# Performance work log

Hardware: AMD Instinct MI355X
Metric: run time of the kernel (lower is better)

The kernel has to match this reference:

```python
import jax, jax.numpy as jnp
import numpy as np

N_NODES = 4194304  # 2**22
LEVELS = 10
COARSE = 8192
RANK = 2
NNZ = 8388608


def _interp_linear(u, N):
    """torch F.interpolate(mode='linear', align_corners=False) along axis 1. u: (B,M,R) -> (B,N,R)."""
    M = u.shape[1]
    pos = (jnp.arange(N, dtype=jnp.float32) + 0.5) * (M / N) - 0.5
    pos = jnp.clip(pos, 0.0, M - 1)
    i0 = jnp.floor(pos).astype(jnp.int32)
    i1 = jnp.minimum(i0 + 1, M - 1)
    w = (pos - i0.astype(jnp.float32))[None, :, None]
    return u[:, i0] * (1.0 - w) + u[:, i1] * w


def _apply_hodlr(diag, u_factors, v_factors, x):
    B, N, _ = x.shape
    y = diag * x
    L = u_factors.shape[0]
    for lvl in range(L):
        num_splits = 2 ** (lvl + 1)
        bs = N // num_splits
        if bs == 0:
            continue
        uc, vc = u_factors[lvl], v_factors[lvl]
        u_full = _interp_linear(uc, N) if uc.shape[1] != N else uc
        v_full = _interp_linear(vc, N) if vc.shape[1] != N else vc
        P = num_splits // 2
        valid = P * 2 * bs
        xv = x[:, :valid].reshape(B, P, 2, bs, 1)
        uv = u_full[:, :valid].reshape(B, P, 2, bs, -1)
        vv = v_full[:, :valid].reshape(B, P, 2, bs, -1)
        xL, xR = xv[:, :, 0], xv[:, :, 1]
        uL, uR = uv[:, :, 0], uv[:, :, 1]
        vL, vR = vv[:, :, 0], vv[:, :, 1]
        xRp = jnp.einsum('bpkr,bpko->bpro', vR, xR)  # (B,P,R,1)
        xLp = jnp.einsum('bpkr,bpko->bpro', vL, xL)
        yL = jnp.einsum('bpkr,bpro->bpko', uL, xRp)  # (B,P,bs,1)
        yR = jnp.einsum('bpkr,bpro->bpko', uR, xLp)
        upd = jnp.stack([yL, yR], axis=2).reshape(B, valid, 1)
        if valid < N:
            upd = jnp.pad(upd, ((0, 0), (0, N - valid), (0, 0)))
        y = y + upd
    return y


def setup_inputs() -> dict:
    key = jax.random.key(0)
    ks = jax.random.split(key, 6)
    diag = jax.random.uniform(ks[0], (1, N_NODES, 1), dtype=jnp.float32)
    u_factors = jax.random.normal(ks[1], (LEVELS, 1, COARSE, RANK), dtype=jnp.float32)
    v_factors = jax.random.normal(ks[2], (LEVELS, 1, COARSE, RANK), dtype=jnp.float32)
    A_values = jax.random.normal(ks[3], (NNZ,), dtype=jnp.float32)
    z = jax.random.normal(ks[4], (1, N_NODES, 1), dtype=jnp.float32)
    A_indices = jax.random.randint(ks[5], (2, NNZ), 0, N_NODES, dtype=jnp.int64) if jax.config.jax_enable_x64 else jax.random.randint(ks[5], (2, NNZ), 0, N_NODES, dtype=jnp.int32)
    return {"diag": diag, "u_factors": u_factors, "v_factors": v_factors,
            "A_values": A_values, "z": z, "A_indices": A_indices, "num_nodes": N_NODES}


def reference(diag, u_factors, v_factors, A_values, z, A_indices, num_nodes):
    N = num_nodes
    w = _apply_hodlr(diag, u_factors, v_factors, z)          # (1,N,1)
    w_flat = w.reshape(N)
    rows, cols = A_indices[0], A_indices[1]
    y_flat = jax.ops.segment_sum(A_values * w_flat[cols], rows, num_segments=N)
    y = y_flat.reshape(1, N, 1)
    loss = jnp.mean((y - z) ** 2)
    return loss
```

## Files before the change

kernel.cpp:

```cpp
#include <hip/hip_runtime.h>

#define N_NODES 4194304
#define LEVELS  10
#define COARSE  8192
#define NNZ_E   8388608
#define NB      256
#define CB_SZ   16384
#define RB_SZ   16384
#define HB      1024
#define EPB     8192
#define TILE    8192
#define CAPC    34816u
#define CAPR    34816u

typedef int          v4i __attribute__((ext_vector_type(4)));
typedef float        v4f __attribute__((ext_vector_type(4)));
typedef unsigned int v4u __attribute__((ext_vector_type(4)));
typedef unsigned int v2u __attribute__((ext_vector_type(2)));

static __device__ __forceinline__ unsigned short f2bf(float x) {
    unsigned u = __float_as_uint(x);
    return (unsigned short)((u + 0x7FFFu + ((u >> 16) & 1u)) >> 16);
}
static __device__ __forceinline__ float bf2f(unsigned short h) {
    return __uint_as_float((unsigned)h << 16);
}
static __device__ __forceinline__ unsigned f18(float p) {
    return ((__float_as_uint(p) + 0x2000u) >> 14) & 0x3FFFFu;
}

__global__ __launch_bounds__(512) void kA(const float* __restrict__ z,
                                          float2* __restrict__ M,
                                          float* __restrict__ S,
                                          float* __restrict__ out,
                                          unsigned* __restrict__ colCtr,
                                          unsigned* __restrict__ rowCtr) {
    int b = blockIdx.x, t = threadIdx.x;
    if (b == 0) {
        for (int i = t; i < 2046 * 2; i += 512) S[i] = 0.f;
        if (t == 0) out[0] = 0.f;
        if (t < 256) {
            colCtr[t] = (unsigned)t * CAPC;
            rowCtr[t] = (unsigned)t * CAPR;
        }
    }
    int lane = t & 63, wave = t >> 6;
    int chunk = b * 8 + wave;
    int base = chunk * 256 + lane * 4;
    float4 zv = *(const float4*)(z + base);
    float a0 = 0.f, a1 = 0.f;
    const float* zp = (const float*)&zv;
#pragma unroll
    for (int j = 0; j < 4; ++j) {
        float p = ((float)(base + j) + 0.5f) * (1.0f / 512.0f) - 0.5f;
        p = fminf(fmaxf(p, 0.0f), (float)(COARSE - 1));
        float f = p - floorf(p);
        a0 += zp[j] * (1.0f - f);
        a1 += zp[j] * f;
    }
#pragma unroll
    for (int off = 32; off >= 1; off >>= 1) {
        a0 += __shfl_xor(a0, off, 64);
        a1 += __shfl_xor(a1, off, 64);
    }
    if (lane == 0) M[chunk] = make_float2(a0, a1);
}

__global__ __launch_bounds__(256) void kB(const float2* __restrict__ M,
                                          const float* __restrict__ V,
                                          float* __restrict__ S) {
    int b = blockIdx.x, t = threadIdx.x;
    int lvl = b >> 3, slice = b & 7;
    const float2* Vl = (const float2*)(V + lvl * COARSE * 2);
    float s0 = 0.f, s1 = 0.f;
    int c0 = slice * 2048 + t * 8;
#pragma unroll
    for (int cc = 0; cc < 8; ++cc) {
        int c = c0 + cc;
        float2 m = M[c];
        int k = (c > 0) ? ((c - 1) >> 1) : 0;
        int kp = min(k + 1, COARSE - 1);
        float2 vk = Vl[k], vkp = Vl[kp];
        s0 += vk.x * m.x + vkp.x * m.y;
        s1 += vk.y * m.x + vkp.y * m.y;
    }
    int gw = min(1 << (10 - lvl), 64);
    for (int sh = gw >> 1; sh >= 1; sh >>= 1) {
        s0 += __shfl_xor(s0, sh, 64);
        s1 += __shfl_xor(s1, sh, 64);
    }
    if ((t & (gw - 1)) == 0) {
        int bb = c0 >> (13 - lvl);
        int soff = (2 << lvl) - 2;
        unsafeAtomicAdd(&S[(soff + bb) * 2 + 0], s0);
        unsafeAtomicAdd(&S[(soff + bb) * 2 + 1], s1);
    }
}

__global__ __launch_bounds__(512) void kC(const float* __restrict__ diag,
                                          const float* __restrict__ z,
                                          const float* __restrict__ S,
                                          const float* __restrict__ U,
                                          unsigned short* __restrict__ wb,
                                          const int* __restrict__ rows,
                                          const int* __restrict__ cols,
                                          const float* __restrict__ vals,
                                          unsigned* __restrict__ colCtr,
                                          v2u* __restrict__ colBinned) {
    int b = blockIdx.x, t = threadIdx.x;
    if (b < 2048) {
        int tid = b * 512 + t;
        int base = tid * 4;
        int c = base >> 8;
        int k = (c > 0) ? ((c - 1) >> 1) : 0;
        int kp = min(k + 1, COARSE - 1);
        float g0 = 0.f, g1 = 0.f;
#pragma unroll
        for (int lvl = 0; lvl < LEVELS; ++lvl) {
            int sib = (c >> (13 - lvl)) ^ 1;
            int soff = (2 << lvl) - 2;
            float2 s2 = ((const float2*)S)[soff + sib];
            const float2* Ul = (const float2*)(U + lvl * COARSE * 2);
            float2 uk = Ul[k], ukp = Ul[kp];
            g0 += uk.x * s2.x + uk.y * s2.y;
            g1 += ukp.x * s2.x + ukp.y * s2.y;
        }
        float4 d4 = *(const float4*)(diag + base);
        float4 z4 = *(const float4*)(z + base);
        const float* dp = (const float*)&d4;
        const float* zp = (const float*)&z4;
        ushort4 h4;
        unsigned short* hp = (unsigned short*)&h4;
#pragma unroll
        for (int j = 0; j < 4; ++j) {
            float p = ((float)(base + j) + 0.5f) * (1.0f / 512.0f) - 0.5f;
            p = fminf(fmaxf(p, 0.0f), (float)(COARSE - 1));
            float f = p - floorf(p);
            hp[j] = f2bf(dp[j] * zp[j] + (g0 + f * (g1 - g0)));
        }
        *(ushort4*)(wb + base) = h4;
    } else {
        __shared__ v2u sortedP[EPB];
        __shared__ unsigned cur[NB], gb[NB];
        __shared__ unsigned wsum[4], wbase[4];
        int blk = b - 2048;
        int base = blk * EPB;
        v4i r[4], c[4];
        v4f v[4];
#pragma unroll
        for (int j = 0; j < 4; ++j) {
            int e = base + j * 2048 + t * 4;
            r[j] = __builtin_nontemporal_load((const v4i*)(rows + e));
            c[j] = __builtin_nontemporal_load((const v4i*)(cols + e));
            v[j] = __builtin_nontemporal_load((const v4f*)(vals + e));
        }
        if (t < 256) cur[t] = 0u;
        __syncthreads();
#pragma unroll
        for (int j = 0; j < 4; ++j) {
            atomicAdd(&cur[c[j].x >> 14], 1u);
            atomicAdd(&cur[c[j].y >> 14], 1u);
            atomicAdd(&cur[c[j].z >> 14], 1u);
            atomicAdd(&cur[c[j].w >> 14], 1u);
        }
        __syncthreads();
        unsigned lv = (t < 256) ? cur[t] : 0u;
        unsigned lincl = lv;
        if (t < 256) {
#pragma unroll
            for (int off = 1; off < 64; off <<= 1) {
                unsigned n = __shfl_up(lincl, off, 64);
                if ((t & 63) >= off) lincl += n;
            }
            if ((t & 63) == 63) wsum[t >> 6] = lincl;
        }
        __syncthreads();
        if (t == 0) {
            unsigned a = 0;
            for (int i = 0; i < 4; ++i) { wbase[i] = a; a += wsum[i]; }
        }
        __syncthreads();
        if (t < 256) {
            unsigned lexcl = wbase[t >> 6] + lincl - lv;
            gb[t] = atomicAdd(&colCtr[t], lv) - lexcl;
            cur[t] = lexcl;
        }
        __syncthreads();
#pragma unroll
        for (int j = 0; j < 4; ++j) {
            const int* rp = (const int*)&r[j];
            const int* cp = (const int*)&c[j];
            const float* vp = (const float*)&v[j];
#pragma unroll
            for (int kk = 0; kk < 4; ++kk) {
                int row = rp[kk], col = cp[kk];
                unsigned cb = (unsigned)col >> 14;
                unsigned cl = (unsigned)col & 16383u;
                v2u ent;
                ent.x = (unsigned)row | ((cl & 0x3FFu) << 22);
                ent.y = (cl >> 10) | (cb << 4) | ((unsigned)f2bf(vp[kk]) << 16);
                unsigned i = atomicAdd(&cur[cb], 1u);
                sortedP[i] = ent;
            }
        }
        __syncthreads();
#pragma unroll
        for (int k = 0; k < 16; ++k) {
            int i = k * 512 + t;
            v2u e = sortedP[i];
            unsigned bkt = (e.y >> 4) & 0xFFu;
            __builtin_nontemporal_store(e, colBinned + gb[bkt] + i);
        }
    }
}

__global__ __launch_bounds__(512) void kD(const unsigned short* __restrict__ wb,
                                          const v2u* __restrict__ colBinned,
                                          const unsigned* __restrict__ colCtr,
                                          unsigned* __restrict__ rowCtr,
                                          unsigned* __restrict__ packed) {
    __shared__ unsigned short wSl[CB_SZ];
    __shared__ unsigned sortedP[TILE];
    __shared__ unsigned char sortedB[TILE];
    __shared__ unsigned cur[NB], gb[NB];
    __shared__ unsigned wsum[4], wbase[4];
    int b = blockIdx.x >> 1, h = blockIdx.x & 1, t = threadIdx.x;

    unsigned s0 = (unsigned)b * CAPC;
    unsigned n = colCtr[b] - s0;
    const v4u* wg = (const v4u*)(wb + (size_t)b * CB_SZ);
    for (int i = t; i < CB_SZ / 8; i += 512) ((v4u*)wSl)[i] = wg[i];
    __syncthreads();

    for (unsigned t0 = (unsigned)h * TILE; t0 < n; t0 += 2u * TILE) {
        unsigned cnt = min((unsigned)TILE, n - t0);
        v2u ev[16];
#pragma unroll
        for (int k = 0; k < 16; ++k) {
            unsigned i = (unsigned)(k * 512 + t);
            if (i < cnt) ev[k] = __builtin_nontemporal_load(colBinned + s0 + t0 + i);
        }
        if (t < 256) cur[t] = 0u;
        __syncthreads();
#pragma unroll
        for (int k = 0; k < 16; ++k) {
            if ((unsigned)(k * 512 + t) < cnt)
                atomicAdd(&cur[(ev[k].x & 0x3FFFFFu) >> 14], 1u);
        }
        __syncthreads();
        unsigned lv = (t < 256) ? cur[t] : 0u;
        unsigned lincl = lv;
        if (t < 256) {
#pragma unroll
            for (int off = 1; off < 64; off <<= 1) {
                unsigned nn = __shfl_up(lincl, off, 64);
                if ((t & 63) >= off) lincl += nn;
            }
            if ((t & 63) == 63) wsum[t >> 6] = lincl;
        }
        __syncthreads();
        if (t == 0) {
            unsigned a = 0;
            for (int i = 0; i < 4; ++i) { wbase[i] = a; a += wsum[i]; }
        }
        __syncthreads();
        if (t < 256) {
            unsigned lexcl = wbase[t >> 6] + lincl - lv;
            gb[t] = atomicAdd(&rowCtr[t], lv) - lexcl;
            cur[t] = lexcl;
        }
        __syncthreads();
#pragma unroll
        for (int k = 0; k < 16; ++k) {
            if ((unsigned)(k * 512 + t) < cnt) {
                v2u e = ev[k];
                unsigned row = e.x & 0x3FFFFFu;
                unsigned cl = (e.x >> 22) | ((e.y & 0xFu) << 10);
                float p = bf2f((unsigned short)(e.y >> 16)) * bf2f(wSl[cl]);
                unsigned rb = row >> 14;
                unsigned i = atomicAdd(&cur[rb], 1u);
                sortedP[i] = ((row & 16383u) << 18) | f18(p);
                sortedB[i] = (unsigned char)rb;
            }
        }
        __syncthreads();
#pragma unroll
        for (int k = 0; k < 16; ++k) {
            unsigned i = (unsigned)(k * 512 + t);
            if (i < cnt) {
                unsigned bkt = sortedB[i];
                __builtin_nontemporal_store(sortedP[i], packed + gb[bkt] + i);
            }
        }
        __syncthreads();
    }
}

__global__ __launch_bounds__(1024) void kE(const unsigned* __restrict__ packed,
                                           const unsigned* __restrict__ rowCtr,
                                           const float* __restrict__ z,
                                           float* __restrict__ out) {
    __shared__ float acc[RB_SZ];
    __shared__ float red[16];
    int b = blockIdx.x, t = threadIdx.x;

    unsigned s0 = (unsigned)b * CAPR;
    unsigned n = rowCtr[b] - s0;
    for (int i = t; i < RB_SZ / 4; i += 1024) ((float4*)acc)[i] = make_float4(0.f, 0.f, 0.f, 0.f);
    __syncthreads();

    for (unsigned i = t; i < n; i += 1024) {
        unsigned e = __builtin_nontemporal_load(packed + s0 + i);
        atomicAdd(&acc[e >> 18], __uint_as_float((e & 0x3FFFFu) << 14));
    }
    __syncthreads();

    float part = 0.f;
    int gbase = b * RB_SZ;
    for (int i = t; i < RB_SZ; i += 1024) {
        float d = acc[i] - z[gbase + i];
        part += d * d;
    }
#pragma unroll
    for (int off = 32; off >= 1; off >>= 1) part += __shfl_xor(part, off, 64);
    if ((t & 63) == 0) red[t >> 6] = part;
    __syncthreads();
    if (t == 0) {
        float s = 0.f;
        for (int i = 0; i < 16; ++i) s += red[i];
        unsafeAtomicAdd(out, s * (1.0f / (float)N_NODES));
    }
}

extern "C" void kernel_launch(void* const* d_in, const int* in_sizes, int n_in,
                              void* d_out, int out_size, void* d_ws, size_t ws_size,
                              hipStream_t stream) {
    const float* diag  = (const float*)d_in[0];
    const float* U     = (const float*)d_in[1];
    const float* V     = (const float*)d_in[2];
    const float* Avals = (const float*)d_in[3];
    const float* z     = (const float*)d_in[4];
    const int*   Aidx  = (const int*)d_in[5];
    const int* rows = Aidx;
    const int* cols = Aidx + NNZ_E;

    char* ws = (char*)d_ws;
    size_t off = 0;
    unsigned short* wb  = (unsigned short*)(ws + off); off += (size_t)N_NODES * 2;
    v2u* colBinned      = (v2u*)(ws + off);            off += (size_t)NB * CAPC * 8;
    unsigned* packed    = (unsigned*)(ws + off);       off += (size_t)NB * CAPR * 4;
    unsigned* colCtr    = (unsigned*)(ws + off);       off += 1024;
    unsigned* rowCtr    = (unsigned*)(ws + off);       off += 1024;
    float2* M           = (float2*)(ws + off);         off += (size_t)(N_NODES / 256) * 8;
    float* S            = (float*)(ws + off);          off += 16384;

    kA<<<2048, 512, 0, stream>>>(z, M, S, (float*)d_out, colCtr, rowCtr);
    kB<<<80, 256, 0, stream>>>(M, V, S);
    kC<<<3072, 512, 0, stream>>>(diag, z, S, U, wb, rows, cols, Avals, colCtr, colBinned);
    kD<<<NB * 2, 512, 0, stream>>>(wb, colBinned, colCtr, rowCtr, packed);
    kE<<<NB, 1024, 0, stream>>>(packed, rowCtr, z, (float*)d_out);
}
```

Baseline: 297.7 us.

## Bin edges by row once and gather w directly in the row-accumulate kernel

```diff
diff --git a/kernel.cpp b/kernel.cpp
--- a/kernel.cpp
+++ b/kernel.cpp
@@ -5,12 +5,8 @@
 #define COARSE  8192
 #define NNZ_E   8388608
 #define NB      256
-#define CB_SZ   16384
 #define RB_SZ   16384
-#define HB      1024
 #define EPB     8192
-#define TILE    8192
-#define CAPC    34816u
 #define CAPR    34816u
 
 typedef int          v4i __attribute__((ext_vector_type(4)));
@@ -25,45 +21,115 @@
 static __device__ __forceinline__ float bf2f(unsigned short h) {
     return __uint_as_float((unsigned)h << 16);
 }
-static __device__ __forceinline__ unsigned f18(float p) {
-    return ((__float_as_uint(p) + 0x2000u) >> 14) & 0x3FFFFu;
-}
 
 __global__ __launch_bounds__(512) void kA(const float* __restrict__ z,
                                           float2* __restrict__ M,
                                           float* __restrict__ S,
                                           float* __restrict__ out,
-                                          unsigned* __restrict__ colCtr,
-                                          unsigned* __restrict__ rowCtr) {
-    int b = blockIdx.x, t = threadIdx.x;
-    if (b == 0) {
-        for (int i = t; i < 2046 * 2; i += 512) S[i] = 0.f;
-        if (t == 0) out[0] = 0.f;
+                                          const int* __restrict__ rows,
+                                          const int* __restrict__ cols,
+                                          const float* __restrict__ vals,
+                                          unsigned* __restrict__ rowCtr,
+                                          v2u* __restrict__ rowBinned) {
+    int b = blockIdx.x, t = threadIdx.x;
+    if (b < 2048) {
+        if (b == 0) {
+            for (int i = t; i < 2046 * 2; i += 512) S[i] = 0.f;
+            if (t == 0) out[0] = 0.f;
+        }
+        int lane = t & 63, wave = t >> 6;
+        int chunk = b * 8 + wave;
+        int base = chunk * 256 + lane * 4;
+        float4 zv = *(const float4*)(z + base);
+        float a0 = 0.f, a1 = 0.f;
+        const float* zp = (const float*)&zv;
+#pragma unroll
+        for (int j = 0; j < 4; ++j) {
+            float p = ((float)(base + j) + 0.5f) * (1.0f / 512.0f) - 0.5f;
+            p = fminf(fmaxf(p, 0.0f), (float)(COARSE - 1));
+            float f = p - floorf(p);
+            a0 += zp[j] * (1.0f - f);
+            a1 += zp[j] * f;
+        }
+#pragma unroll
+        for (int off = 32; off >= 1; off >>= 1) {
+            a0 += __shfl_xor(a0, off, 64);
+            a1 += __shfl_xor(a1, off, 64);
+        }
+        if (lane == 0) M[chunk] = make_float2(a0, a1);
+    } else {
+        __shared__ v2u sortedP[EPB];
+        __shared__ unsigned cur[NB], gb[NB];
+        __shared__ unsigned wsum[4], wbase[4];
+        int blk = b - 2048;
+        int base = blk * EPB;
+        v4i r[4], c[4];
+        v4f v[4];
+#pragma unroll
+        for (int j = 0; j < 4; ++j) {
+            int e = base + j * 2048 + t * 4;
+            r[j] = __builtin_nontemporal_load((const v4i*)(rows + e));
+            c[j] = __builtin_nontemporal_load((const v4i*)(cols + e));
+            v[j] = __builtin_nontemporal_load((const v4f*)(vals + e));
+        }
+        if (t < 256) cur[t] = 0u;
+        __syncthreads();
+#pragma unroll
+        for (int j = 0; j < 4; ++j) {
+            atomicAdd(&cur[(unsigned)r[j].x >> 14], 1u);
+            atomicAdd(&cur[(unsigned)r[j].y >> 14], 1u);
+            atomicAdd(&cur[(unsigned)r[j].z >> 14], 1u);
+            atomicAdd(&cur[(unsigned)r[j].w >> 14], 1u);
+        }
+        __syncthreads();
+        unsigned lv = (t < 256) ? cur[t] : 0u;
+        unsigned lincl = lv;
         if (t < 256) {
-            colCtr[t] = (unsigned)t * CAPC;
-            rowCtr[t] = (unsigned)t * CAPR;
-        }
-    }
-    int lane = t & 63, wave = t >> 6;
-    int chunk = b * 8 + wave;
-    int base = chunk * 256 + lane * 4;
-    float4 zv = *(const float4*)(z + base);
-    float a0 = 0.f, a1 = 0.f;
-    const float* zp = (const float*)&zv;
-#pragma unroll
-    for (int j = 0; j < 4; ++j) {
-        float p = ((float)(base + j) + 0.5f) * (1.0f / 512.0f) - 0.5f;
-        p = fminf(fmaxf(p, 0.0f), (float)(COARSE - 1));
-        float f = p - floorf(p);
-        a0 += zp[j] * (1.0f - f);
-        a1 += zp[j] * f;
-    }
-#pragma unroll
-    for (int off = 32; off >= 1; off >>= 1) {
-        a0 += __shfl_xor(a0, off, 64);
-        a1 += __shfl_xor(a1, off, 64);
-    }
-    if (lane == 0) M[chunk] = make_float2(a0, a1);
+#pragma unroll
+            for (int off = 1; off < 64; off <<= 1) {
+                unsigned n = __shfl_up(lincl, off, 64);
+                if ((t & 63) >= off) lincl += n;
+            }
+            if ((t & 63) == 63) wsum[t >> 6] = lincl;
+        }
+        __syncthreads();
+        if (t == 0) {
+            unsigned a = 0;
+            for (int i = 0; i < 4; ++i) { wbase[i] = a; a += wsum[i]; }
+        }
+        __syncthreads();
+        if (t < 256) {
+            unsigned lexcl = wbase[t >> 6] + lincl - lv;
+            gb[t] = (unsigned)t * CAPR + atomicAdd(&rowCtr[t], lv) - lexcl;
+            cur[t] = lexcl;
+        }
+        __syncthreads();
+#pragma unroll
+        for (int j = 0; j < 4; ++j) {
+            const int* rp = (const int*)&r[j];
+            const int* cp = (const int*)&c[j];
+            const float* vp = (const float*)&v[j];
+#pragma unroll
+            for (int kk = 0; kk < 4; ++kk) {
+                unsigned row = (unsigned)rp[kk], col = (unsigned)cp[kk];
+                unsigned rb = row >> 14;
+                unsigned rl = row & 16383u;
+                v2u ent;
+                ent.x = col | ((rl & 0x3FFu) << 22);
+                ent.y = (rl >> 10) | (rb << 4) | ((unsigned)f2bf(vp[kk]) << 16);
+                unsigned i = atomicAdd(&cur[rb], 1u);
+                sortedP[i] = ent;
+            }
+        }
+        __syncthreads();
+#pragma unroll
+        for (int k = 0; k < 16; ++k) {
+            int i = k * 512 + t;
+            v2u e = sortedP[i];
+            unsigned bkt = (e.y >> 4) & 0xFFu;
+            __builtin_nontemporal_store(e, rowBinned + gb[bkt] + i);
+        }
+    }
 }
 
 __global__ __launch_bounds__(256) void kB(const float2* __restrict__ M,
@@ -97,228 +163,87 @@
     }
 }
 
-__global__ __launch_bounds__(512) void kC(const float* __restrict__ diag,
-                                          const float* __restrict__ z,
-                                          const float* __restrict__ S,
-                                          const float* __restrict__ U,
-                                          unsigned short* __restrict__ wb,
-                                          const int* __restrict__ rows,
-                                          const int* __restrict__ cols,
-                                          const float* __restrict__ vals,
-                                          unsigned* __restrict__ colCtr,
-                                          v2u* __restrict__ colBinned) {
-    int b = blockIdx.x, t = threadIdx.x;
-    if (b < 2048) {
-        int tid = b * 512 + t;
-        int base = tid * 4;
-        int c = base >> 8;
-        int k = (c > 0) ? ((c - 1) >> 1) : 0;
-        int kp = min(k + 1, COARSE - 1);
-        float g0 = 0.f, g1 = 0.f;
-#pragma unroll
-        for (int lvl = 0; lvl < LEVELS; ++lvl) {
-            int sib = (c >> (13 - lvl)) ^ 1;
-            int soff = (2 << lvl) - 2;
-            float2 s2 = ((const float2*)S)[soff + sib];
-            const float2* Ul = (const float2*)(U + lvl * COARSE * 2);
-            float2 uk = Ul[k], ukp = Ul[kp];
-            g0 += uk.x * s2.x + uk.y * s2.y;
-            g1 += ukp.x * s2.x + ukp.y * s2.y;
-        }
-        float4 d4 = *(const float4*)(diag + base);
-        float4 z4 = *(const float4*)(z + base);
-        const float* dp = (const float*)&d4;
-        const float* zp = (const float*)&z4;
-        ushort4 h4;
-        unsigned short* hp = (unsigned short*)&h4;
-#pragma unroll
-        for (int j = 0; j < 4; ++j) {
-            float p = ((float)(base + j) + 0.5f) * (1.0f / 512.0f) - 0.5f;
-            p = fminf(fmaxf(p, 0.0f), (float)(COARSE - 1));
-            float f = p - floorf(p);
-            hp[j] = f2bf(dp[j] * zp[j] + (g0 + f * (g1 - g0)));
-        }
-        *(ushort4*)(wb + base) = h4;
-    } else {
-        __shared__ v2u sortedP[EPB];
-        __shared__ unsigned cur[NB], gb[NB];
-        __shared__ unsigned wsum[4], wbase[4];
-        int blk = b - 2048;
-        int base = blk * EPB;
-        v4i r[4], c[4];
-        v4f v[4];
-#pragma unroll
-        for (int j = 0; j < 4; ++j) {
-            int e = base + j * 2048 + t * 4;
-            r[j] = __builtin_nontemporal_load((const v4i*)(rows + e));
-            c[j] = __builtin_nontemporal_load((const v4i*)(cols + e));
-            v[j] = __builtin_nontemporal_load((const v4f*)(vals + e));
-        }
-        if (t < 256) cur[t] = 0u;
-        __syncthreads();
-#pragma unroll
-        for (int j = 0; j < 4; ++j) {
-            atomicAdd(&cur[c[j].x >> 14], 1u);
-            atomicAdd(&cur[c[j].y >> 14], 1u);
-            atomicAdd(&cur[c[j].z >> 14], 1u);
-            atomicAdd(&cur[c[j].w >> 14], 1u);
-        }
-        __syncthreads();
-        unsigned lv = (t < 256) ? cur[t] : 0u;
-        unsigned lincl = lv;
-        if (t < 256) {
-#pragma unroll
-            for (int off = 1; off < 64; off <<= 1) {
-                unsigned n = __shfl_up(lincl, off, 64);
-                if ((t & 63) >= off) lincl += n;
-            }
-            if ((t & 63) == 63) wsum[t >> 6] = lincl;
-        }
-        __syncthreads();
-        if (t == 0) {
-            unsigned a = 0;
-            for (int i = 0; i < 4; ++i) { wbase[i] = a; a += wsum[i]; }
-        }
-        __syncthreads();
-        if (t < 256) {
-            unsigned lexcl = wbase[t >> 6] + lincl - lv;
-            gb[t] = atomicAdd(&colCtr[t], lv) - lexcl;
-            cur[t] = lexcl;
-        }
-        __syncthreads();
-#pragma unroll
-        for (int j = 0; j < 4; ++j) {
-            const int* rp = (const int*)&r[j];
-            const int* cp = (const int*)&c[j];
-            const float* vp = (const float*)&v[j];
-#pragma unroll
-            for (int kk = 0; kk < 4; ++kk) {
-                int row = rp[kk], col = cp[kk];
-                unsigned cb = (unsigned)col >> 14;
-                unsigned cl = (unsigned)col & 16383u;
-                v2u ent;
-                ent.x = (unsigned)row | ((cl & 0x3FFu) << 22);
-                ent.y = (cl >> 10) | (cb << 4) | ((unsigned)f2bf(vp[kk]) << 16);
-                unsigned i = atomicAdd(&cur[cb], 1u);
-                sortedP[i] = ent;
-            }
-        }
-        __syncthreads();
-#pragma unroll
-        for (int k = 0; k < 16; ++k) {
-            int i = k * 512 + t;
-            v2u e = sortedP[i];
-            unsigned bkt = (e.y >> 4) & 0xFFu;
-            __builtin_nontemporal_store(e, colBinned + gb[bkt] + i);
-        }
-    }
-}
-
-__global__ __launch_bounds__(512) void kD(const unsigned short* __restrict__ wb,
-                                          const v2u* __restrict__ colBinned,
-                                          const unsigned* __restrict__ colCtr,
-                                          unsigned* __restrict__ rowCtr,
-                                          unsigned* __restrict__ packed) {
-    __shared__ unsigned short wSl[CB_SZ];
-    __shared__ unsigned sortedP[TILE];
-    __shared__ unsigned char sortedB[TILE];
-    __shared__ unsigned cur[NB], gb[NB];
-    __shared__ unsigned wsum[4], wbase[4];
-    int b = blockIdx.x >> 1, h = blockIdx.x & 1, t = threadIdx.x;
-
-    unsigned s0 = (unsigned)b * CAPC;
-    unsigned n = colCtr[b] - s0;
-    const v4u* wg = (const v4u*)(wb + (size_t)b * CB_SZ);
-    for (int i = t; i < CB_SZ / 8; i += 512) ((v4u*)wSl)[i] = wg[i];
-    __syncthreads();
-
-    for (unsigned t0 = (unsigned)h * TILE; t0 < n; t0 += 2u * TILE) {
-        unsigned cnt = min((unsigned)TILE, n - t0);
-        v2u ev[16];
-#pragma unroll
-        for (int k = 0; k < 16; ++k) {
-            unsigned i = (unsigned)(k * 512 + t);
-            if (i < cnt) ev[k] = __builtin_nontemporal_load(colBinned + s0 + t0 + i);
-        }
-        if (t < 256) cur[t] = 0u;
-        __syncthreads();
-#pragma unroll
-        for (int k = 0; k < 16; ++k) {
-            if ((unsigned)(k * 512 + t) < cnt)
-                atomicAdd(&cur[(ev[k].x & 0x3FFFFFu) >> 14], 1u);
-        }
-        __syncthreads();
-        unsigned lv = (t < 256) ? cur[t] : 0u;
-        unsigned lincl = lv;
-        if (t < 256) {
-#pragma unroll
-            for (int off = 1; off < 64; off <<= 1) {
-                unsigned nn = __shfl_up(lincl, off, 64);
-                if ((t & 63) >= off) lincl += nn;
-            }
-            if ((t & 63) == 63) wsum[t >> 6] = lincl;
-        }
-        __syncthreads();
-        if (t == 0) {
-            unsigned a = 0;
-            for (int i = 0; i < 4; ++i) { wbase[i] = a; a += wsum[i]; }
-        }
-        __syncthreads();
-        if (t < 256) {
-            unsigned lexcl = wbase[t >> 6] + lincl - lv;
-            gb[t] = atomicAdd(&rowCtr[t], lv) - lexcl;
-            cur[t] = lexcl;
-        }
-        __syncthreads();
-#pragma unroll
-        for (int k = 0; k < 16; ++k) {
-            if ((unsigned)(k * 512 + t) < cnt) {
-                v2u e = ev[k];
-                unsigned row = e.x & 0x3FFFFFu;
-                unsigned cl = (e.x >> 22) | ((e.y & 0xFu) << 10);
-                float p = bf2f((unsigned short)(e.y >> 16)) * bf2f(wSl[cl]);
-                unsigned rb = row >> 14;
-                unsigned i = atomicAdd(&cur[rb], 1u);
-                sortedP[i] = ((row & 16383u) << 18) | f18(p);
-                sortedB[i] = (unsigned char)rb;
-            }
-        }
-        __syncthreads();
-#pragma unroll
-        for (int k = 0; k < 16; ++k) {
-            unsigned i = (unsigned)(k * 512 + t);
-            if (i < cnt) {
-                unsigned bkt = sortedB[i];
-                __builtin_nontemporal_store(sortedP[i], packed + gb[bkt] + i);
-            }
-        }
-        __syncthreads();
-    }
-}
-
-__global__ __launch_bounds__(1024) void kE(const unsigned* __restrict__ packed,
+__global__ __launch_bounds__(512) void kCw(const float* __restrict__ diag,
+                                           const float* __restrict__ z,
+                                           const float* __restrict__ S,
+                                           const float* __restrict__ U,
+                                           unsigned short* __restrict__ wb) {
+    int b = blockIdx.x, t = threadIdx.x;
+    int tid = b * 512 + t;
+    int base = tid * 4;
+    int c = base >> 8;
+    int k = (c > 0) ? ((c - 1) >> 1) : 0;
+    int kp = min(k + 1, COARSE - 1);
+    float g0 = 0.f, g1 = 0.f;
+#pragma unroll
+    for (int lvl = 0; lvl < LEVELS; ++lvl) {
+        int sib = (c >> (13 - lvl)) ^ 1;
+        int soff = (2 << lvl) - 2;
+        float2 s2 = ((const float2*)S)[soff + sib];
+        const float2* Ul = (const float2*)(U + lvl * COARSE * 2);
+        float2 uk = Ul[k], ukp = Ul[kp];
+        g0 += uk.x * s2.x + uk.y * s2.y;
+        g1 += ukp.x * s2.x + ukp.y * s2.y;
+    }
+    float4 d4 = *(const float4*)(diag + base);
+    float4 z4 = *(const float4*)(z + base);
+    const float* dp = (const float*)&d4;
+    const float* zp = (const float*)&z4;
+    ushort4 h4;
+    unsigned short* hp = (unsigned short*)&h4;
+#pragma unroll
+    for (int j = 0; j < 4; ++j) {
+        float p = ((float)(base + j) + 0.5f) * (1.0f / 512.0f) - 0.5f;
+        p = fminf(fmaxf(p, 0.0f), (float)(COARSE - 1));
+        float f = p - floorf(p);
+        hp[j] = f2bf(dp[j] * zp[j] + (g0 + f * (g1 - g0)));
+    }
+    *(ushort4*)(wb + base) = h4;
+}
+
+__global__ __launch_bounds__(1024) void kE(const v2u* __restrict__ rowBinned,
                                            const unsigned* __restrict__ rowCtr,
+                                           const unsigned short* __restrict__ wb,
                                            const float* __restrict__ z,
                                            float* __restrict__ out) {
     __shared__ float acc[RB_SZ];
     __shared__ float red[16];
     int b = blockIdx.x, t = threadIdx.x;
 
-    unsigned s0 = (unsigned)b * CAPR;
-    unsigned n = rowCtr[b] - s0;
+    unsigned n = rowCtr[b];
+    const v2u* seg = rowBinned + (size_t)b * CAPR;
     for (int i = t; i < RB_SZ / 4; i += 1024) ((float4*)acc)[i] = make_float4(0.f, 0.f, 0.f, 0.f);
     __syncthreads();
 
-    for (unsigned i = t; i < n; i += 1024) {
-        unsigned e = __builtin_nontemporal_load(packed + s0 + i);
-        atomicAdd(&acc[e >> 18], __uint_as_float((e & 0x3FFFFu) << 14));
+    unsigned i = t;
+    for (; i + 7u * 1024u < n; i += 8u * 1024u) {
+        v2u ev[8];
+#pragma unroll
+        for (int k = 0; k < 8; ++k)
+            ev[k] = __builtin_nontemporal_load(seg + i + (unsigned)k * 1024u);
+        unsigned short wv[8];
+#pragma unroll
+        for (int k = 0; k < 8; ++k)
+            wv[k] = wb[ev[k].x & 0x3FFFFFu];
+#pragma unroll
+        for (int k = 0; k < 8; ++k) {
+            unsigned rl = (ev[k].x >> 22) | ((ev[k].y & 0xFu) << 10);
+            float p = bf2f((unsigned short)(ev[k].y >> 16)) * bf2f(wv[k]);
+            atomicAdd(&acc[rl], p);
+        }
+    }
+    for (; i < n; i += 1024u) {
+        v2u e = __builtin_nontemporal_load(seg + i);
+        unsigned rl = (e.x >> 22) | ((e.y & 0xFu) << 10);
+        float p = bf2f((unsigned short)(e.y >> 16)) * bf2f(wb[e.x & 0x3FFFFFu]);
+        atomicAdd(&acc[rl], p);
     }
     __syncthreads();
 
     float part = 0.f;
     int gbase = b * RB_SZ;
-    for (int i = t; i < RB_SZ; i += 1024) {
-        float d = acc[i] - z[gbase + i];
+    for (int k = t; k < RB_SZ; k += 1024) {
+        float d = acc[k] - z[gbase + k];
         part += d * d;
     }
 #pragma unroll
@@ -327,7 +252,7 @@
     __syncthreads();
     if (t == 0) {
         float s = 0.f;
-        for (int i = 0; i < 16; ++i) s += red[i];
+        for (int k = 0; k < 16; ++k) s += red[k];
         unsafeAtomicAdd(out, s * (1.0f / (float)N_NODES));
     }
 }
@@ -347,16 +272,14 @@
     char* ws = (char*)d_ws;
     size_t off = 0;
     unsigned short* wb  = (unsigned short*)(ws + off); off += (size_t)N_NODES * 2;
-    v2u* colBinned      = (v2u*)(ws + off);            off += (size_t)NB * CAPC * 8;
-    unsigned* packed    = (unsigned*)(ws + off);       off += (size_t)NB * CAPR * 4;
-    unsigned* colCtr    = (unsigned*)(ws + off);       off += 1024;
+    v2u* rowBinned      = (v2u*)(ws + off);            off += (size_t)NB * CAPR * 8;
     unsigned* rowCtr    = (unsigned*)(ws + off);       off += 1024;
     float2* M           = (float2*)(ws + off);         off += (size_t)(N_NODES / 256) * 8;
     float* S            = (float*)(ws + off);          off += 16384;
 
-    kA<<<2048, 512, 0, stream>>>(z, M, S, (float*)d_out, colCtr, rowCtr);
+    hipMemsetAsync(rowCtr, 0, NB * 4, stream);
+    kA<<<3072, 512, 0, stream>>>(z, M, S, (float*)d_out, rows, cols, Avals, rowCtr, rowBinned);
     kB<<<80, 256, 0, stream>>>(M, V, S);
-    kC<<<3072, 512, 0, stream>>>(diag, z, S, U, wb, rows, cols, Avals, colCtr, colBinned);
-    kD<<<NB * 2, 512, 0, stream>>>(wb, colBinned, colCtr, rowCtr, packed);
-    kE<<<NB, 1024, 0, stream>>>(packed, rowCtr, z, (float*)d_out);
-}
+    kCw<<<2048, 512, 0, stream>>>(diag, z, S, U, wb);
+    kE<<<NB, 1024, 0, stream>>>(rowBinned, rowCtr, wb, z, (float*)d_out);
+}
```

After: 294.9 us. Within noise of the previous version (-0.9%).
